# Kernel tuning notes

Hardware: AMD Instinct MI355X
Metric: run time of the kernel (lower is better)

The kernel has to match this reference:

```python
import jax, jax.numpy as jnp
import numpy as np

N_IN = 100000
N_OUT = 5000
N_EDGES = 200000
FILTERS = 4
BATCH = 128


def setup_inputs() -> dict:
    key = jax.random.key(0)
    k1, k2, k3, k4 = jax.random.split(key, 4)
    x = jax.random.normal(k1, (BATCH, N_IN), dtype=jnp.float32)
    weight = jax.random.normal(k2, (N_EDGES, FILTERS), dtype=jnp.float32) * 0.01
    bias = jnp.zeros((N_OUT, FILTERS), dtype=jnp.float32)
    rows = jax.random.randint(k3, (N_EDGES,), 0, N_IN)
    cols = jax.random.randint(k4, (N_EDGES,), 0, N_OUT)
    return {"x": x, "weight": weight, "bias": bias, "rows": rows, "cols": cols}


def reference(x, weight, bias, rows, cols):
    # Sparse locally-connected layer: out[b,o,f] = sum_{e: cols[e]==o} x[b, rows[e]] * weight[e, f]
    # (equivalent to the original dense einsum 'bi,iof->bof' with the scattered weight tensor,
    #  but computed directly on the COO edge list)
    xg = x[:, rows]                                   # (B, E) gather per edge
    contrib = xg[:, :, None] * weight[None, :, :]     # (B, E, F)
    out = jnp.zeros((x.shape[0], N_OUT, FILTERS), dtype=x.dtype)
    out = out.at[:, cols, :].add(contrib)             # scatter-add to output nodes
    out = out + bias[None, :, :]
    return jax.nn.relu(out)
```

## Files before the change

kernel.cpp:

```cpp
#include <hip/hip_runtime.h>

#define N_IN 100000
#define N_OUT 5000
#define N_EDGES 200000
#define NB 128
#define CAP 128
#define T_TILES 3125
#define S_BLOCKS 782
#define LDSW 132
#define POISON 0xAAAAAAAAu

__device__ __forceinline__ unsigned short f2bf_rne(float f) {
    unsigned int u = __float_as_uint(f);
    u += 0x7FFF + ((u >> 16) & 1);
    return (unsigned short)(u >> 16);
}

__device__ __forceinline__ void ld_step(unsigned int u, unsigned int w01, unsigned int w23,
                                        float4& a0, float4& a1) {
    float xa = __uint_as_float(u << 16);
    float xb = __uint_as_float(u & 0xFFFF0000u);
    float wx = __uint_as_float(w01 << 16);
    float wy = __uint_as_float(w01 & 0xFFFF0000u);
    float wz = __uint_as_float(w23 << 16);
    float ww = __uint_as_float(w23 & 0xFFFF0000u);
    a0.x = fmaf(xa, wx, a0.x); a0.y = fmaf(xa, wy, a0.y);
    a0.z = fmaf(xa, wz, a0.z); a0.w = fmaf(xa, ww, a0.w);
    a1.x = fmaf(xb, wx, a1.x); a1.y = fmaf(xb, wy, a1.y);
    a1.z = fmaf(xb, wz, a1.z); a1.w = fmaf(xb, ww, a1.w);
}

__global__ __launch_bounds__(256) void fused_prep(
    const float* __restrict__ x, unsigned short* __restrict__ xTb,
    const int* __restrict__ rows, const int* __restrict__ cols,
    const float4* __restrict__ w4,
    unsigned int* __restrict__ count, int4* __restrict__ edge_pack) {
    __shared__ float tile[32][LDSW];
    int t = threadIdx.x;
    if (blockIdx.x < T_TILES) {
        int n0 = blockIdx.x * 32;
        int q = t & 7;
        int brow = t >> 3;
#pragma unroll
        for (int p = 0; p < 4; ++p) {
            int b = brow + 32 * p;
            float4 v = *(const float4*)(x + (size_t)b * N_IN + n0 + 4 * q);
            tile[4 * q + 0][b] = v.x;
            tile[4 * q + 1][b] = v.y;
            tile[4 * q + 2][b] = v.z;
            tile[4 * q + 3][b] = v.w;
        }
        __syncthreads();
        int s = t & 31;
        int r = t >> 5;
#pragma unroll
        for (int p = 0; p < 4; ++p) {
            int nl = r + 8 * p;
            float4 f = *(const float4*)&tile[nl][4 * s];
            ushort4 o;
            o.x = f2bf_rne(f.x);
            o.y = f2bf_rne(f.y);
            o.z = f2bf_rne(f.z);
            o.w = f2bf_rne(f.w);
            *(ushort4*)(xTb + (size_t)(n0 + nl) * NB + 4 * s) = o;
        }
    } else {
        int e = (blockIdx.x - T_TILES) * 256 + t;
        if (e < N_EDGES) {
            int c = cols[e];
            unsigned int pos = atomicAdd(&count[c], 1u) - POISON;
            if (pos < CAP) {
                float4 w = w4[e];
                unsigned int w01 = (unsigned int)f2bf_rne(w.x) |
                                   ((unsigned int)f2bf_rne(w.y) << 16);
                unsigned int w23 = (unsigned int)f2bf_rne(w.z) |
                                   ((unsigned int)f2bf_rne(w.w) << 16);
                edge_pack[c * CAP + pos] = make_int4(rows[e] << 8, (int)w01, (int)w23, 0);
            }
        }
    }
}

__global__ __launch_bounds__(256) void ld1d_main(
    const char* __restrict__ xgc,
    const float4* __restrict__ bias4,
    const unsigned int* __restrict__ count, const int4* __restrict__ edge_pack,
    float4* __restrict__ out4) {
    __shared__ int4 s_pack[4][CAP];
    int t = threadIdx.x;
    int wv = t >> 6;
    int l = t & 63;
    int c = blockIdx.x * 4 + wv;
    unsigned int cu = count[c] - POISON;
    int cnt = (cu < CAP) ? (int)cu : CAP;
    int cntp = (cnt + 7) & ~7;
    if (l < cnt) s_pack[wv][l] = edge_pack[c * CAP + l];
    else if (l < cntp) s_pack[wv][l] = make_int4(0, 0, 0, 0);
    if (l + 64 < cnt) s_pack[wv][l + 64] = edge_pack[c * CAP + l + 64];
    else if (l + 64 < cntp) s_pack[wv][l + 64] = make_int4(0, 0, 0, 0);
    float4 a0 = bias4[c];
    float4 a1 = a0;
    unsigned int lb = (unsigned int)(l << 2);
    for (int k = 0; k < cntp; k += 8) {
        int4 p0 = s_pack[wv][k],     p1 = s_pack[wv][k + 1];
        int4 p2 = s_pack[wv][k + 2], p3 = s_pack[wv][k + 3];
        int4 p4 = s_pack[wv][k + 4], p5 = s_pack[wv][k + 5];
        int4 p6 = s_pack[wv][k + 6], p7 = s_pack[wv][k + 7];
        unsigned int u0 = *(const unsigned int*)(xgc + ((unsigned int)p0.x + lb));
        unsigned int u1 = *(const unsigned int*)(xgc + ((unsigned int)p1.x + lb));
        unsigned int u2 = *(const unsigned int*)(xgc + ((unsigned int)p2.x + lb));
        unsigned int u3 = *(const unsigned int*)(xgc + ((unsigned int)p3.x + lb));
        unsigned int u4 = *(const unsigned int*)(xgc + ((unsigned int)p4.x + lb));
        unsigned int u5 = *(const unsigned int*)(xgc + ((unsigned int)p5.x + lb));
        unsigned int u6 = *(const unsigned int*)(xgc + ((unsigned int)p6.x + lb));
        unsigned int u7 = *(const unsigned int*)(xgc + ((unsigned int)p7.x + lb));
        ld_step(u0, (unsigned int)p0.y, (unsigned int)p0.z, a0, a1);
        ld_step(u1, (unsigned int)p1.y, (unsigned int)p1.z, a0, a1);
        ld_step(u2, (unsigned int)p2.y, (unsigned int)p2.z, a0, a1);
        ld_step(u3, (unsigned int)p3.y, (unsigned int)p3.z, a0, a1);
        ld_step(u4, (unsigned int)p4.y, (unsigned int)p4.z, a0, a1);
        ld_step(u5, (unsigned int)p5.y, (unsigned int)p5.z, a0, a1);
        ld_step(u6, (unsigned int)p6.y, (unsigned int)p6.z, a0, a1);
        ld_step(u7, (unsigned int)p7.y, (unsigned int)p7.z, a0, a1);
    }
    a0.x = fmaxf(a0.x, 0.f); a0.y = fmaxf(a0.y, 0.f);
    a0.z = fmaxf(a0.z, 0.f); a0.w = fmaxf(a0.w, 0.f);
    a1.x = fmaxf(a1.x, 0.f); a1.y = fmaxf(a1.y, 0.f);
    a1.z = fmaxf(a1.z, 0.f); a1.w = fmaxf(a1.w, 0.f);
    out4[(size_t)(2 * l) * N_OUT + c] = a0;
    out4[(size_t)(2 * l + 1) * N_OUT + c] = a1;
}

extern "C" void kernel_launch(void* const* d_in, const int* in_sizes, int n_in,
                              void* d_out, int out_size, void* d_ws, size_t ws_size,
                              hipStream_t stream) {
    const float* x      = (const float*)d_in[0];
    const float* weight = (const float*)d_in[1];
    const float* bias   = (const float*)d_in[2];
    const int*   rows   = (const int*)d_in[3];
    const int*   cols   = (const int*)d_in[4];

    char* ws = (char*)d_ws;
    unsigned short* xTb = (unsigned short*)(ws + 0);
    int4* edge_pack = (int4*)(ws + 25600000);
    unsigned int* count = (unsigned int*)(ws + 35840000);

    fused_prep<<<T_TILES + S_BLOCKS, 256, 0, stream>>>(x, xTb, rows, cols,
                                                       (const float4*)weight, count, edge_pack);

    ld1d_main<<<N_OUT / 4, 256, 0, stream>>>((const char*)xTb, (const float4*)bias,
                                             count, edge_pack, (float4*)d_out);
}
```

Baseline: 121.0 us.

## Coarsen transpose blocks, schedule scatter blocks first, use packed bf16 convert

Each transpose block now processes four 32-column tiles instead of one, which cuts the block count and amortizes launch and scheduling overhead. The next tile's loads are issued before the barrier. Scatter blocks are placed first so the atomic edge binning starts early. Float-to-bf16 conversion uses the hardware packed convert instruction instead of manual rounding. The trade-off is fewer blocks, which may reduce memory-level parallelism, plus extra barriers per block.

```diff
diff --git a/kernel.cpp b/kernel.cpp
--- a/kernel.cpp
+++ b/kernel.cpp
@@ -5,15 +5,15 @@
 #define N_EDGES 200000
 #define NB 128
 #define CAP 128
-#define T_TILES 3125
 #define S_BLOCKS 782
+#define T_BLOCKS 782
 #define LDSW 132
 #define POISON 0xAAAAAAAAu
 
-__device__ __forceinline__ unsigned short f2bf_rne(float f) {
-    unsigned int u = __float_as_uint(f);
-    u += 0x7FFF + ((u >> 16) & 1);
-    return (unsigned short)(u >> 16);
+__device__ __forceinline__ unsigned int cvt_pk_bf16(float lo, float hi) {
+    unsigned int r;
+    asm("v_cvt_pk_bf16_f32 %0, %1, %2" : "=v"(r) : "v"(lo), "v"(hi));
+    return r;
 }
 
 __device__ __forceinline__ void ld_step(unsigned int u, unsigned int w01, unsigned int w23,
@@ -37,45 +37,50 @@
     unsigned int* __restrict__ count, int4* __restrict__ edge_pack) {
     __shared__ float tile[32][LDSW];
     int t = threadIdx.x;
-    if (blockIdx.x < T_TILES) {
-        int n0 = blockIdx.x * 32;
-        int q = t & 7;
-        int brow = t >> 3;
-#pragma unroll
-        for (int p = 0; p < 4; ++p) {
-            int b = brow + 32 * p;
-            float4 v = *(const float4*)(x + (size_t)b * N_IN + n0 + 4 * q);
-            tile[4 * q + 0][b] = v.x;
-            tile[4 * q + 1][b] = v.y;
-            tile[4 * q + 2][b] = v.z;
-            tile[4 * q + 3][b] = v.w;
-        }
-        __syncthreads();
-        int s = t & 31;
-        int r = t >> 5;
-#pragma unroll
-        for (int p = 0; p < 4; ++p) {
-            int nl = r + 8 * p;
-            float4 f = *(const float4*)&tile[nl][4 * s];
-            ushort4 o;
-            o.x = f2bf_rne(f.x);
-            o.y = f2bf_rne(f.y);
-            o.z = f2bf_rne(f.z);
-            o.w = f2bf_rne(f.w);
-            *(ushort4*)(xTb + (size_t)(n0 + nl) * NB + 4 * s) = o;
-        }
-    } else {
-        int e = (blockIdx.x - T_TILES) * 256 + t;
+    if (blockIdx.x < S_BLOCKS) {
+        int e = blockIdx.x * 256 + t;
         if (e < N_EDGES) {
             int c = cols[e];
             unsigned int pos = atomicAdd(&count[c], 1u) - POISON;
             if (pos < CAP) {
                 float4 w = w4[e];
-                unsigned int w01 = (unsigned int)f2bf_rne(w.x) |
-                                   ((unsigned int)f2bf_rne(w.y) << 16);
-                unsigned int w23 = (unsigned int)f2bf_rne(w.z) |
-                                   ((unsigned int)f2bf_rne(w.w) << 16);
+                unsigned int w01 = cvt_pk_bf16(w.x, w.y);
+                unsigned int w23 = cvt_pk_bf16(w.z, w.w);
                 edge_pack[c * CAP + pos] = make_int4(rows[e] << 8, (int)w01, (int)w23, 0);
+            }
+        }
+    } else {
+        int tb = blockIdx.x - S_BLOCKS;
+        int q = t & 7;
+        int brow = t >> 3;
+        int s = t & 31;
+        int r = t >> 5;
+#pragma unroll
+        for (int p2 = 0; p2 < 4; ++p2) {
+            int n0 = tb * 128 + p2 * 32;
+            if (n0 >= N_IN) break;
+            float4 v[4];
+#pragma unroll
+            for (int p = 0; p < 4; ++p)
+                v[p] = *(const float4*)(x + (size_t)(brow + 32 * p) * N_IN + n0 + 4 * q);
+            __syncthreads();
+#pragma unroll
+            for (int p = 0; p < 4; ++p) {
+                int b = brow + 32 * p;
+                tile[4 * q + 0][b] = v[p].x;
+                tile[4 * q + 1][b] = v[p].y;
+                tile[4 * q + 2][b] = v[p].z;
+                tile[4 * q + 3][b] = v[p].w;
+            }
+            __syncthreads();
+#pragma unroll
+            for (int p = 0; p < 4; ++p) {
+                int nl = r + 8 * p;
+                float4 f = *(const float4*)&tile[nl][4 * s];
+                uint2 o;
+                o.x = cvt_pk_bf16(f.x, f.y);
+                o.y = cvt_pk_bf16(f.z, f.w);
+                *(uint2*)(xTb + (size_t)(n0 + nl) * NB + 4 * s) = o;
             }
         }
     }
@@ -145,8 +150,8 @@
     int4* edge_pack = (int4*)(ws + 25600000);
     unsigned int* count = (unsigned int*)(ws + 35840000);
 
-    fused_prep<<<T_TILES + S_BLOCKS, 256, 0, stream>>>(x, xTb, rows, cols,
-                                                       (const float4*)weight, count, edge_pack);
+    fused_prep<<<S_BLOCKS + T_BLOCKS, 256, 0, stream>>>(x, xTb, rows, cols,
+                                                        (const float4*)weight, count, edge_pack);
 
     ld1d_main<<<N_OUT / 4, 256, 0, stream>>>((const char*)xTb, (const float4*)bias,
                                              count, edge_pack, (float4*)d_out);
```

Result: slower. 127.0 us (+4.9%).
